# Optimization experiments

Measured on AMD Instinct MI355X. Metric: run time of the kernel, lower is better.

Reference implementation:

```python
import jax, jax.numpy as jnp
import numpy as np
from jax import lax

B, T, D = 8, 4096, 512
UNITS = 512
WINDOW = 2


def setup_inputs() -> dict:
    key = jax.random.key(0)
    k1, k2, k3 = jax.random.split(key, 3)
    x = jax.random.normal(k1, (B, T, D), dtype=jnp.float32)
    # keras kernel shape is (window, 1, input_dim, 3*units); drop the dummy height dim
    kernel = jax.random.uniform(k2, (WINDOW, D, 3 * UNITS), dtype=jnp.float32,
                                minval=-0.05, maxval=0.05)
    bias = jnp.zeros((3 * UNITS,), dtype=jnp.float32)
    return {"x": x, "kernel": kernel, "bias": bias}


def reference(x, kernel, bias):
    window, d_in, u3 = kernel.shape
    units = u3 // 3
    # causal padding: window-1 zeros on the left of the time axis
    xp = jnp.pad(x, ((0, 0), (window - 1, 0), (0, 0)))
    # 1D valid conv -> gates [B, T, 3*units]
    gates = lax.conv_general_dilated(
        xp, kernel, window_strides=(1,), padding='VALID',
        dimension_numbers=('NWC', 'WIO', 'NWC')) + bias
    z = jnp.tanh(gates[..., :units])
    f = jax.nn.sigmoid(gates[..., units:2 * units])
    o = jax.nn.sigmoid(gates[..., 2 * units:])

    # fo-pool recurrence: c_t = f_t * c_{t-1} + (1 - f_t) * z_t ; out_t = o_t * c_t
    def step(c, zfo):
        z_t, f_t, o_t = zfo
        c = f_t * c + (1.0 - f_t) * z_t
        return c, o_t * c

    c0 = jnp.zeros((x.shape[0], units), dtype=x.dtype)
    zT = jnp.swapaxes(z, 0, 1)  # [T, B, U]
    fT = jnp.swapaxes(f, 0, 1)
    oT = jnp.swapaxes(o, 0, 1)
    _, ysT = lax.scan(step, c0, (zT, fT, oT))
    return jnp.swapaxes(ysT, 0, 1)  # [B, T, U] (return_sequences=True)
```

## Files before the change

kernel.cpp:

```cpp
#include <hip/hip_runtime.h>
#include <cstdint>
#include <cstddef>

#define BB   8
#define TT   4096
#define DD   512
#define UU   512
#define NN   1536
#define KK   1024
#define MM   32768
#define NCH  256
#define CHL  16

using bf16x8 = __attribute__((ext_vector_type(8))) __bf16;
using f32x4  = __attribute__((ext_vector_type(4))) float;
using us8    = __attribute__((ext_vector_type(8))) unsigned short;

__device__ __forceinline__ unsigned short f2bf(float f) {
    unsigned u = __float_as_uint(f);
    u += 0x7fffu + ((u >> 16) & 1u);
    return (unsigned short)(u >> 16);
}
__device__ __forceinline__ float bf2f(unsigned short s) {
    return __uint_as_float(((unsigned)s) << 16);
}
__device__ __forceinline__ float sigf(float x) { return 1.0f / (1.0f + __expf(-x)); }
__device__ __forceinline__ float tanh_(float x) { return 1.0f - 2.0f / (1.0f + __expf(2.0f * x)); }

__device__ __forceinline__ void async16(const void* g, void* l) {
    __builtin_amdgcn_global_load_lds(
        (__attribute__((address_space(1))) void*)g,
        (__attribute__((address_space(3))) void*)l, 16, 0, 0);
}

__global__ void k_prep(const float* __restrict__ x, unsigned short* __restrict__ xpad,
                       const float* __restrict__ kern, unsigned short* __restrict__ kT) {
    int bx = blockIdx.x;
    int by = blockIdx.y;
    int tid = threadIdx.x;
    if (bx < 1025) {
        int q = bx * 256 + tid;
        if (q >= 4097 * 64) return;
        int tp = q >> 6;
        int d  = (q & 63) << 3;
        size_t oi = ((size_t)by * 4097 + tp) * 512 + d;
        us8 o;
        if (tp == 0) {
            o = (us8)0;
        } else {
            const float* src = x + ((size_t)by * 4096 + (tp - 1)) * 512 + d;
            float4 v0 = *(const float4*)(src);
            float4 v1 = *(const float4*)(src + 4);
            o[0] = f2bf(v0.x); o[1] = f2bf(v0.y); o[2] = f2bf(v0.z); o[3] = f2bf(v0.w);
            o[4] = f2bf(v1.x); o[5] = f2bf(v1.y); o[6] = f2bf(v1.z); o[7] = f2bf(v1.w);
        }
        *(us8*)(xpad + oi) = o;
    } else {
        __shared__ float tile[32][33];
        int idx = (bx - 1025) * 8 + by;
        int c  = tid & 31;
        int r0 = tid >> 5;
        for (int t8 = 0; t8 < 8; ++t8) {
            int tnum = idx * 8 + t8;
            int k0 = (tnum & 31) * 32;
            int n0 = (tnum >> 5) * 32;
#pragma unroll
            for (int rr = r0; rr < 32; rr += 8)
                tile[rr][c] = kern[(size_t)(k0 + rr) * NN + n0 + c];
            __syncthreads();
#pragma unroll
            for (int rr = r0; rr < 32; rr += 8)
                kT[(size_t)(n0 + rr) * KK + k0 + c] = f2bf(tile[c][rr]);
            __syncthreads();
        }
    }
}

__global__ __launch_bounds__(256) void k_gemm(
    const unsigned short* __restrict__ xpad,
    const unsigned short* __restrict__ kT,
    const float* __restrict__ bias,
    unsigned short* __restrict__ gates)
{
    __shared__ unsigned short As[128 * 64];
    __shared__ unsigned short Bs[128 * 64];
    const int tid  = threadIdx.x;
    const int bi   = blockIdx.x;
    const int xcd  = bi & 7;
    const int loc  = bi >> 3;
    const int mt   = xcd * 32 + loc / 12;
    const int nt   = loc % 12;
    const int m0   = mt * 128;
    const int n0   = nt * 128;
    const int boff = m0 >> 12;
    const size_t abase = (size_t)(m0 + boff) * 512;

    f32x4 acc[4][4] = {};

    const int wid  = tid >> 6;
    const int lane = tid & 63;
    const int wm   = (wid & 1) * 64;
    const int wn   = (wid >> 1) * 64;
    const int lrow = lane & 15;
    const int quad = lane >> 4;

    for (int kk = 0; kk < KK; kk += 64) {
#pragma unroll
        for (int q = 0; q < 4; ++q) {
            int L   = q * 256 + tid;
            int row = L >> 3;
            int sp  = L & 7;
            int sl  = sp ^ (row & 7);
            async16(xpad + abase + (size_t)row * 512 + kk + sl * 8, As + (size_t)L * 8);
            async16(kT + (size_t)(n0 + row) * KK + kk + sl * 8, Bs + (size_t)L * 8);
        }
        __syncthreads();
#pragma unroll
        for (int ks = 0; ks < 2; ++ks) {
            bf16x8 af[4], bfr[4];
#pragma unroll
            for (int i = 0; i < 4; ++i) {
                int row = wm + i * 16 + lrow;
                int sp  = (ks * 4 + quad) ^ (row & 7);
                af[i] = *(const bf16x8*)(As + row * 64 + sp * 8);
            }
#pragma unroll
            for (int j = 0; j < 4; ++j) {
                int row = wn + j * 16 + lrow;
                int sp  = (ks * 4 + quad) ^ (row & 7);
                bfr[j] = *(const bf16x8*)(Bs + row * 64 + sp * 8);
            }
#pragma unroll
            for (int i = 0; i < 4; ++i)
#pragma unroll
                for (int j = 0; j < 4; ++j)
                    acc[i][j] = __builtin_amdgcn_mfma_f32_16x16x32_bf16(af[i], bfr[j], acc[i][j], 0, 0, 0);
        }
        __syncthreads();
    }

#pragma unroll
    for (int j = 0; j < 4; ++j) {
        int col  = n0 + wn + j * 16 + lrow;
        float bv = bias[col];
#pragma unroll
        for (int i = 0; i < 4; ++i) {
            int rbase = m0 + wm + i * 16 + quad * 4;
#pragma unroll
            for (int r = 0; r < 4; ++r) {
                gates[(size_t)(rbase + r) * NN + col] = f2bf(acc[i][j][r] + bv);
            }
        }
    }
}

__global__ __launch_bounds__(256) void k_scanA(const unsigned short* __restrict__ gates,
                        float* __restrict__ Fp, float* __restrict__ Ce) {
    const int wave  = threadIdx.x >> 6;
    const int lane  = threadIdx.x & 63;
    const int chunk = blockIdx.x * 4 + wave;
    const int b     = blockIdx.y;
    const int u     = lane << 3;
    const size_t g0 = ((size_t)b * TT + (size_t)chunk * CHL) * NN + u;

    float c[8] = {0, 0, 0, 0, 0, 0, 0, 0};
    float F[8] = {1, 1, 1, 1, 1, 1, 1, 1};

    us8 bz[4], bf_[4];
#pragma unroll
    for (int j = 0; j < 4; ++j) {
        bz[j]  = *(const us8*)(gates + g0 + (size_t)j * NN);
        bf_[j] = *(const us8*)(gates + g0 + (size_t)j * NN + UU);
    }
#pragma unroll
    for (int k = 0; k < 4; ++k) {
        us8 nz[4], nf[4];
        if (k < 3) {
#pragma unroll
            for (int j = 0; j < 4; ++j) {
                size_t gg = g0 + (size_t)((k + 1) * 4 + j) * NN;
                nz[j] = *(const us8*)(gates + gg);
                nf[j] = *(const us8*)(gates + gg + UU);
            }
        }
#pragma unroll
        for (int j = 0; j < 4; ++j) {
#pragma unroll
            for (int e = 0; e < 8; ++e) {
                float f = sigf(bf2f(bf_[j][e]));
                float z = tanh_(bf2f(bz[j][e]));
                c[e] = f * c[e] + (1.0f - f) * z;
                F[e] *= f;
            }
        }
        if (k < 3) {
#pragma unroll
            for (int j = 0; j < 4; ++j) { bz[j] = nz[j]; bf_[j] = nf[j]; }
        }
    }
    size_t ci = ((size_t)b * NCH + chunk) * UU + u;
    *(f32x4*)(Fp + ci)     = f32x4{F[0], F[1], F[2], F[3]};
    *(f32x4*)(Fp + ci + 4) = f32x4{F[4], F[5], F[6], F[7]};
    *(f32x4*)(Ce + ci)     = f32x4{c[0], c[1], c[2], c[3]};
    *(f32x4*)(Ce + ci + 4) = f32x4{c[4], c[5], c[6], c[7]};
}

__global__ __launch_bounds__(128) void k_scanB(const float* __restrict__ Fp,
                        const float* __restrict__ Ce, float* __restrict__ Cin) {
    int gid = blockIdx.x * 128 + threadIdx.x;
    int bb = gid >> 9;
    int uu = gid & 511;
    size_t base = (size_t)bb * NCH * UU + uu;
    float c = 0.0f;
    for (int k0 = 0; k0 < NCH; k0 += 8) {
        float F[8], E[8];
#pragma unroll
        for (int j = 0; j < 8; ++j) {
            F[j] = Fp[base + (size_t)(k0 + j) * UU];
            E[j] = Ce[base + (size_t)(k0 + j) * UU];
        }
#pragma unroll
        for (int j = 0; j < 8; ++j) {
            Cin[base + (size_t)(k0 + j) * UU] = c;
            c = F[j] * c + E[j];
        }
    }
}

__global__ __launch_bounds__(256) void k_scanC(const unsigned short* __restrict__ gates,
                        const float* __restrict__ Cin, float* __restrict__ out) {
    const int wave  = threadIdx.x >> 6;
    const int lane  = threadIdx.x & 63;
    const int chunk = blockIdx.x * 4 + wave;
    const int b     = blockIdx.y;
    const int u     = lane << 3;
    const size_t g0 = ((size_t)b * TT + (size_t)chunk * CHL) * NN + u;
    size_t o = ((size_t)b * TT + (size_t)chunk * CHL) * UU + u;

    size_t ci = ((size_t)b * NCH + chunk) * UU + u;
    float c[8];
    {
        f32x4 cv0 = *(const f32x4*)(Cin + ci);
        f32x4 cv1 = *(const f32x4*)(Cin + ci + 4);
        c[0] = cv0[0]; c[1] = cv0[1]; c[2] = cv0[2]; c[3] = cv0[3];
        c[4] = cv1[0]; c[5] = cv1[1]; c[6] = cv1[2]; c[7] = cv1[3];
    }

    us8 bz[4], bf_[4], bo[4];
#pragma unroll
    for (int j = 0; j < 4; ++j) {
        bz[j]  = *(const us8*)(gates + g0 + (size_t)j * NN);
        bf_[j] = *(const us8*)(gates + g0 + (size_t)j * NN + UU);
        bo[j]  = *(const us8*)(gates + g0 + (size_t)j * NN + 2 * UU);
    }
#pragma unroll
    for (int k = 0; k < 4; ++k) {
        us8 nz[4], nf[4], no[4];
        if (k < 3) {
#pragma unroll
            for (int j = 0; j < 4; ++j) {
                size_t gg = g0 + (size_t)((k + 1) * 4 + j) * NN;
                nz[j] = *(const us8*)(gates + gg);
                nf[j] = *(const us8*)(gates + gg + UU);
                no[j] = *(const us8*)(gates + gg + 2 * UU);
            }
        }
#pragma unroll
        for (int j = 0; j < 4; ++j) {
            float y[8];
#pragma unroll
            for (int e = 0; e < 8; ++e) {
                float f  = sigf(bf2f(bf_[j][e]));
                float z  = tanh_(bf2f(bz[j][e]));
                float og = sigf(bf2f(bo[j][e]));
                c[e] = f * c[e] + (1.0f - f) * z;
                y[e] = og * c[e];
            }
            f32x4 y0 = {y[0], y[1], y[2], y[3]};
            f32x4 y1 = {y[4], y[5], y[6], y[7]};
            __builtin_nontemporal_store(y0, (f32x4*)(out + o));
            __builtin_nontemporal_store(y1, (f32x4*)(out + o + 4));
            o += UU;
        }
        if (k < 3) {
#pragma unroll
            for (int j = 0; j < 4; ++j) { bz[j] = nz[j]; bf_[j] = nf[j]; bo[j] = no[j]; }
        }
    }
}

extern "C" void kernel_launch(void* const* d_in, const int* in_sizes, int n_in,
                              void* d_out, int out_size, void* d_ws, size_t ws_size,
                              hipStream_t stream) {
    const float* x    = (const float*)d_in[0];
    const float* kern = (const float*)d_in[1];
    const float* bias = (const float*)d_in[2];
    float* out = (float*)d_out;
    char* ws = (char*)d_ws;

    unsigned short* xpad  = (unsigned short*)(ws + 0);
    unsigned short* kT    = (unsigned short*)(ws + 33562624);
    unsigned short* gates = (unsigned short*)(ws + 36708352);
    float* Fp  = (float*)(ws + 137371648);
    float* Ce  = (float*)(ws + 141565952);
    float* Cin = (float*)(ws + 145760256);

    hipLaunchKernelGGL(k_prep,  dim3(1025 + 24, 8), dim3(256), 0, stream, x, xpad, kern, kT);
    hipLaunchKernelGGL(k_gemm,  dim3(3072),         dim3(256), 0, stream, xpad, kT, bias, gates);
    hipLaunchKernelGGL(k_scanA, dim3(NCH / 4, BB),  dim3(256), 0, stream, gates, Fp, Ce);
    hipLaunchKernelGGL(k_scanB, dim3(32),           dim3(128), 0, stream, Fp, Ce, Cin);
    hipLaunchKernelGGL(k_scanC, dim3(NCH / 4, BB),  dim3(256), 0, stream, gates, Cin, out);
}
```

Measured before the change: 327.7 us.

## Fuse x fp32-to-bf16 conversion and causal padding into GEMM A-tile loads

Drops the separate prep pass that wrote a padded bf16 copy of x. The GEMM now reads fp32 x directly, converts it to bf16 in registers (using the packed convert builtin when available) and writes the A tile to LDS. The zero row for causal padding is handled with a predicate. This saves a full read+write pass over x, but the A loads become synchronous register loads instead of async global-to-LDS, and the fp32 reads double the bytes fetched per tile, with each x tile read by 12 N-tile blocks.

```diff
diff --git a/kernel.cpp b/kernel.cpp
--- a/kernel.cpp
+++ b/kernel.cpp
@@ -27,57 +27,40 @@
 __device__ __forceinline__ float sigf(float x) { return 1.0f / (1.0f + __expf(-x)); }
 __device__ __forceinline__ float tanh_(float x) { return 1.0f - 2.0f / (1.0f + __expf(2.0f * x)); }
 
+#if __has_builtin(__builtin_amdgcn_cvt_pk_bf16_f32)
+__device__ __forceinline__ void cvt2(unsigned short* dst, float a, float b) {
+    auto r = __builtin_amdgcn_cvt_pk_bf16_f32(a, b);
+    __builtin_memcpy(dst, &r, 4);
+}
+#else
+__device__ __forceinline__ void cvt2(unsigned short* dst, float a, float b) {
+    dst[0] = f2bf(a); dst[1] = f2bf(b);
+}
+#endif
+
 __device__ __forceinline__ void async16(const void* g, void* l) {
     __builtin_amdgcn_global_load_lds(
         (__attribute__((address_space(1))) void*)g,
         (__attribute__((address_space(3))) void*)l, 16, 0, 0);
 }
 
-__global__ void k_prep(const float* __restrict__ x, unsigned short* __restrict__ xpad,
-                       const float* __restrict__ kern, unsigned short* __restrict__ kT) {
-    int bx = blockIdx.x;
-    int by = blockIdx.y;
-    int tid = threadIdx.x;
-    if (bx < 1025) {
-        int q = bx * 256 + tid;
-        if (q >= 4097 * 64) return;
-        int tp = q >> 6;
-        int d  = (q & 63) << 3;
-        size_t oi = ((size_t)by * 4097 + tp) * 512 + d;
-        us8 o;
-        if (tp == 0) {
-            o = (us8)0;
-        } else {
-            const float* src = x + ((size_t)by * 4096 + (tp - 1)) * 512 + d;
-            float4 v0 = *(const float4*)(src);
-            float4 v1 = *(const float4*)(src + 4);
-            o[0] = f2bf(v0.x); o[1] = f2bf(v0.y); o[2] = f2bf(v0.z); o[3] = f2bf(v0.w);
-            o[4] = f2bf(v1.x); o[5] = f2bf(v1.y); o[6] = f2bf(v1.z); o[7] = f2bf(v1.w);
-        }
-        *(us8*)(xpad + oi) = o;
-    } else {
-        __shared__ float tile[32][33];
-        int idx = (bx - 1025) * 8 + by;
-        int c  = tid & 31;
-        int r0 = tid >> 5;
-        for (int t8 = 0; t8 < 8; ++t8) {
-            int tnum = idx * 8 + t8;
-            int k0 = (tnum & 31) * 32;
-            int n0 = (tnum >> 5) * 32;
-#pragma unroll
-            for (int rr = r0; rr < 32; rr += 8)
-                tile[rr][c] = kern[(size_t)(k0 + rr) * NN + n0 + c];
-            __syncthreads();
-#pragma unroll
-            for (int rr = r0; rr < 32; rr += 8)
-                kT[(size_t)(n0 + rr) * KK + k0 + c] = f2bf(tile[c][rr]);
-            __syncthreads();
-        }
-    }
+__global__ void k_tr(const float* __restrict__ kern, unsigned short* __restrict__ kT) {
+    __shared__ float tile[32][33];
+    int k0 = blockIdx.x * 32;
+    int n0 = blockIdx.y * 32;
+    int c  = threadIdx.x & 31;
+    int r0 = threadIdx.x >> 5;
+#pragma unroll
+    for (int rr = r0; rr < 32; rr += 8)
+        tile[rr][c] = kern[(size_t)(k0 + rr) * NN + n0 + c];
+    __syncthreads();
+#pragma unroll
+    for (int rr = r0; rr < 32; rr += 8)
+        kT[(size_t)(n0 + rr) * KK + k0 + c] = f2bf(tile[c][rr]);
 }
 
 __global__ __launch_bounds__(256) void k_gemm(
-    const unsigned short* __restrict__ xpad,
+    const float* __restrict__ x,
     const unsigned short* __restrict__ kT,
     const float* __restrict__ bias,
     unsigned short* __restrict__ gates)
@@ -92,8 +75,7 @@
     const int nt   = loc % 12;
     const int m0   = mt * 128;
     const int n0   = nt * 128;
-    const int boff = m0 >> 12;
-    const size_t abase = (size_t)(m0 + boff) * 512;
+    const int t0   = m0 & 4095;
 
     f32x4 acc[4][4] = {};
 
@@ -111,8 +93,27 @@
             int row = L >> 3;
             int sp  = L & 7;
             int sl  = sp ^ (row & 7);
-            async16(xpad + abase + (size_t)row * 512 + kk + sl * 8, As + (size_t)L * 8);
             async16(kT + (size_t)(n0 + row) * KK + kk + sl * 8, Bs + (size_t)L * 8);
+        }
+#pragma unroll
+        for (int q = 0; q < 4; ++q) {
+            int L    = q * 256 + tid;
+            int row  = L >> 3;
+            int sp   = L & 7;
+            int sl   = sp ^ (row & 7);
+            int koff = kk + sl * 8;
+            unsigned short tmp[8];
+            if (t0 + row == 0 && koff < 512) {
+#pragma unroll
+                for (int e = 0; e < 8; ++e) tmp[e] = 0;
+            } else {
+                const float* s = x + (size_t)(m0 + row + (koff >> 9) - 1) * 512 + (koff & 511);
+                float4 v0 = *(const float4*)(s);
+                float4 v1 = *(const float4*)(s + 4);
+                cvt2(tmp + 0, v0.x, v0.y); cvt2(tmp + 2, v0.z, v0.w);
+                cvt2(tmp + 4, v1.x, v1.y); cvt2(tmp + 6, v1.z, v1.w);
+            }
+            *(us8*)(As + (size_t)L * 8) = *(const us8*)tmp;
         }
         __syncthreads();
 #pragma unroll
@@ -298,16 +299,15 @@
     float* out = (float*)d_out;
     char* ws = (char*)d_ws;
 
-    unsigned short* xpad  = (unsigned short*)(ws + 0);
-    unsigned short* kT    = (unsigned short*)(ws + 33562624);
-    unsigned short* gates = (unsigned short*)(ws + 36708352);
-    float* Fp  = (float*)(ws + 137371648);
-    float* Ce  = (float*)(ws + 141565952);
-    float* Cin = (float*)(ws + 145760256);
-
-    hipLaunchKernelGGL(k_prep,  dim3(1025 + 24, 8), dim3(256), 0, stream, x, xpad, kern, kT);
-    hipLaunchKernelGGL(k_gemm,  dim3(3072),         dim3(256), 0, stream, xpad, kT, bias, gates);
-    hipLaunchKernelGGL(k_scanA, dim3(NCH / 4, BB),  dim3(256), 0, stream, gates, Fp, Ce);
-    hipLaunchKernelGGL(k_scanB, dim3(32),           dim3(128), 0, stream, Fp, Ce, Cin);
-    hipLaunchKernelGGL(k_scanC, dim3(NCH / 4, BB),  dim3(256), 0, stream, gates, Cin, out);
-}
+    unsigned short* kT    = (unsigned short*)(ws + 0);
+    unsigned short* gates = (unsigned short*)(ws + 3145728);
+    float* Fp  = (float*)(ws + 103809024);
+    float* Ce  = (float*)(ws + 108003328);
+    float* Cin = (float*)(ws + 112197632);
+
+    hipLaunchKernelGGL(k_tr,    dim3(32, 48),      dim3(256), 0, stream, kern, kT);
+    hipLaunchKernelGGL(k_gemm,  dim3(3072),        dim3(256), 0, stream, x, kT, bias, gates);
+    hipLaunchKernelGGL(k_scanA, dim3(NCH / 4, BB), dim3(256), 0, stream, gates, Fp, Ce);
+    hipLaunchKernelGGL(k_scanB, dim3(32),          dim3(128), 0, stream, Fp, Ce, Cin);
+    hipLaunchKernelGGL(k_scanC, dim3(NCH / 4, BB), dim3(256), 0, stream, gates, Cin, out);
+}
```

New measurement: 330.0 us. No clear change (+0.7%).
